# Kernel optimization log

Measured on AMD Instinct MI355X. Metric: run time of the kernel, lower is better.

The kernel has to match this reference:

```python
import jax, jax.numpy as jnp
import numpy as np

N, E, F, H, O, B = 100000, 1200000, 64, 1024, 1, 256


def _gcn_conv(x, W, b, src, dst, ew, num_nodes):
    # PyG GCNConv: out_i = sum_{(s->i)} d_i^{-1/2} w_e d_s^{-1/2} (x_s W) + b
    deg = jax.ops.segment_sum(ew, dst, num_segments=num_nodes)
    dinv = jnp.where(deg > 0, jax.lax.rsqrt(jnp.maximum(deg, 1e-12)), 0.0)
    norm = dinv[src] * ew * dinv[dst]          # [E]
    h = x @ W                                   # [N, out]
    msg = h[src] * norm[:, None]                # gather + scale
    return jax.ops.segment_sum(msg, dst, num_segments=num_nodes) + b


def setup_inputs() -> dict:
    key = jax.random.key(0)
    ks = jax.random.split(key, 12)
    def lin(k, fan_in, fan_out):
        s = 1.0 / np.sqrt(fan_in)
        kw, kb = jax.random.split(k)
        return (jax.random.uniform(kw, (fan_in, fan_out), jnp.float32, -s, s),
                jax.random.uniform(kb, (fan_out,), jnp.float32, -s, s))
    W1, b1 = lin(ks[0], F, F)
    W2, b2 = lin(ks[1], F, 2 * F)
    W3, b3 = lin(ks[2], 2 * F, 4 * F)
    Wf1, bf1 = lin(ks[3], 5 * F, H)
    Wf2, bf2 = lin(ks[4], H, O)
    feature = jax.random.normal(ks[5], (N, F), jnp.float32)
    edge_index = jax.random.randint(ks[6], (2, E), 0, N, jnp.int32)
    weight = jax.random.uniform(ks[7], (E,), jnp.float32)
    protein_batch = jnp.sort(jax.random.randint(ks[8], (N,), 0, B, jnp.int32))
    return {"feature": feature, "edge_index": edge_index, "weight": weight,
            "protein_batch": protein_batch,
            "W1": W1, "b1": b1, "W2": W2, "b2": b2, "W3": W3, "b3": b3,
            "Wf1": Wf1, "bf1": bf1, "Wf2": Wf2, "bf2": bf2}


def reference(feature, edge_index, weight, protein_batch,
              W1, b1, W2, b2, W3, b3, Wf1, bf1, Wf2, bf2):
    num_nodes = feature.shape[0]
    # add self-loops with weight 1 (PyG default)
    loop = jnp.arange(num_nodes, dtype=edge_index.dtype)
    src = jnp.concatenate([edge_index[0], loop])
    dst = jnp.concatenate([edge_index[1], loop])
    ew = jnp.concatenate([weight, jnp.ones((num_nodes,), weight.dtype)])

    x = jax.nn.relu(_gcn_conv(feature, W1, b1, src, dst, ew, num_nodes))
    x = jax.nn.relu(_gcn_conv(x, W2, b2, src, dst, ew, num_nodes))
    x = jax.nn.relu(_gcn_conv(x, W3, b3, src, dst, ew, num_nodes))
    x = jnp.concatenate([x, feature], axis=1)   # [N, 5F]

    # global_mean_pool over graph ids
    sums = jax.ops.segment_sum(x, protein_batch, num_segments=B)
    cnts = jax.ops.segment_sum(jnp.ones((num_nodes,), x.dtype), protein_batch, num_segments=B)
    gc = sums / jnp.maximum(cnts, 1.0)[:, None]

    gc = jax.nn.relu(gc @ Wf1 + bf1)            # dropout is identity in eval
    return gc @ Wf2 + bf2
```

## Files before the change

kernel.cpp:

```cpp
#include <hip/hip_runtime.h>
#include <cstdio>
#include <cstdint>

typedef _Float16 f16x8 __attribute__((ext_vector_type(8)));
typedef float f32x4 __attribute__((ext_vector_type(4)));

__device__ inline unsigned short f2bf(float f) {
  unsigned u = __float_as_uint(f);
  u += 0x7fffu + ((u >> 16) & 1u);
  return (unsigned short)(u >> 16);
}
__device__ inline float bf2f(unsigned short h) {
  return __uint_as_float(((unsigned)h) << 16);
}
__device__ inline unsigned short f2h(float f) {
  union { _Float16 h; unsigned short u; } cv;
  cv.h = (_Float16)f;
  return cv.u;
}

#define EPB 4096


__global__ __launch_bounds__(256)
void k_prep0(float* __restrict__ psum,
             const float* __restrict__ feature, ushort* __restrict__ featb,
             const float* __restrict__ W1, ushort* __restrict__ w1h,
             const float* __restrict__ W2, ushort* __restrict__ w2h,
             const float* __restrict__ W3, ushort* __restrict__ w3h,
             const int* __restrict__ pb, int* __restrict__ gs,
             const int* __restrict__ dst, int* __restrict__ H,
             int* __restrict__ rs,
             int BC, int NF, int F, int D2, int D3,
             int N, int B, int NB, int E,
             int nB, int nC, int nD, int nG) {
  __shared__ int hist[512];
  int b = blockIdx.x;
  int t = threadIdx.x;
  if (b < nB) {
    int i = b * 256 + t;
    if (i < BC) psum[i] = 0.f;
  } else if (b < nB + nC) {
    int base = ((b - nB) * 256 + t) * 4;
    if (base < NF) {
      float4 v = *reinterpret_cast<const float4*>(feature + base);
      ushort4 h;
      h.x = f2bf(v.x); h.y = f2bf(v.y); h.z = f2bf(v.z); h.w = f2bf(v.w);
      *reinterpret_cast<ushort4*>(featb + base) = h;
    }
  } else if (b < nB + nC + nD) {
    int idx = (b - nB - nC) * 256 + t;
    int s1 = F * F, s2 = s1 + F * D2, s3 = s2 + D2 * D3;
    if (idx < s1) {
      int k = idx / F, n = idx - k * F;
      w1h[(size_t)n * F + k] = f2h(W1[idx]);
    } else if (idx < s2) {
      int i2 = idx - s1; int k = i2 / D2, n = i2 - k * D2;
      w2h[(size_t)n * F + k] = f2h(W2[i2]);
    } else if (idx < s3) {
      int i3 = idx - s2; int k = i3 / D3, n = i3 - k * D3;
      w3h[(size_t)n * D2 + k] = f2h(W3[i3]);
    }
  } else if (b < nB + nC + nD + nG) {
    int bb = (b - nB - nC - nD) * 256 + t;
    if (bb == 0) rs[N] = E;
    if (bb <= B) {
      int lo = 0, hi = N;
      while (lo < hi) {
        int mid = (lo + hi) >> 1;
        if (pb[mid] < bb) lo = mid + 1; else hi = mid;
      }
      gs[bb] = lo;
    }
  } else {
    const int bi = b - nB - nC - nD - nG;
    for (int i = t; i < NB; i += 256) hist[i] = 0;
    __syncthreads();
    const int base = bi * EPB + t;
#pragma unroll
    for (int j = 0; j < EPB / 256; j++) {
      int e = base + 256 * j;
      if (e < E) atomicAdd(&hist[dst[e] >> 8], 1);
    }
    __syncthreads();
    for (int i = t; i < NB; i += 256) H[(size_t)bi * NB + i] = hist[i];
  }
}

__global__ __launch_bounds__(256)
void k_bscan1(const int* __restrict__ H, int* __restrict__ S,
              int* __restrict__ bsum, int NB, int NBLK, int T) {
  __shared__ int sh[256];
  const int t = threadIdx.x;
  const int base = blockIdx.x * 1024;
  int v[4]; int s = 0;
#pragma unroll
  for (int j = 0; j < 4; j++) {
    int idx = base + t * 4 + j;
    if (idx < T) {
      int bin = idx / NBLK, bi = idx - bin * NBLK;
      v[j] = H[(size_t)bi * NB + bin];
    } else v[j] = 0;
    s += v[j];
  }
  sh[t] = s;
  __syncthreads();
  for (int off = 1; off < 256; off <<= 1) {
    int x = (t >= off) ? sh[t - off] : 0;
    __syncthreads();
    sh[t] += x;
    __syncthreads();
  }
  int run = sh[t] - s;
#pragma unroll
  for (int j = 0; j < 4; j++) {
    int idx = base + t * 4 + j;
    if (idx < T) S[idx] = run;
    run += v[j];
  }
  if (t == 255) bsum[blockIdx.x] = sh[255];
}

__device__ inline void build_prefix(const int* __restrict__ bsum, int nch,
                                    int* __restrict__ pre, int t) {
  for (int i = t; i < nch; i += 256) pre[i] = bsum[i];
  __syncthreads();
  if (t == 0) {
    int run = 0;
    for (int i = 0; i < nch; i++) { int v = pre[i]; pre[i] = run; run += v; }
  }
  __syncthreads();
}

__global__ __launch_bounds__(256)
void k_bscatter(const int* __restrict__ src, const int* __restrict__ dst,
                const float* __restrict__ ew, const int* __restrict__ S,
                const int* __restrict__ bsb,
                int* __restrict__ sdst, int2* __restrict__ ssw,
                int NB, int NBLK, int E, int nchT) {
  __shared__ int cnt[512];
  __shared__ int sbase[512];
  __shared__ int pre[512];
  const int t = threadIdx.x, bi = blockIdx.x;
  build_prefix(bsb, nchT, pre, t);
  for (int i = t; i < NB; i += 256) {
    cnt[i] = 0;
    int j = i * NBLK + bi;
    sbase[i] = S[j] + pre[j >> 10];
  }
  __syncthreads();
  const int base = bi * EPB + t;
#pragma unroll
  for (int j = 0; j < EPB / 256; j++) {
    int e = base + 256 * j;
    if (e < E) {
      int d = dst[e];
      int bin = d >> 8;
      int r = atomicAdd(&cnt[bin], 1);
      int pos = sbase[bin] + r;
      sdst[pos] = d;
      ssw[pos] = make_int2(src[e], __float_as_int(ew[e]));
    }
  }
}

__global__ __launch_bounds__(256)
void k_bprocA(const int* __restrict__ sdst, const int2* __restrict__ ssw,
              const int* __restrict__ S, const int* __restrict__ bsb,
              int* __restrict__ cntN, float* __restrict__ wsumN,
              int NB, int NBLK, int N, int E, int nchT) {
  __shared__ int cnt[256];
  __shared__ float wsm[256];
  __shared__ int pre[512];
  const int t = threadIdx.x, bin = blockIdx.x;
  build_prefix(bsb, nchT, pre, t);
  cnt[t] = 0; wsm[t] = 0.f;
  __syncthreads();
  int j0 = bin * NBLK;
  const int start = S[j0] + pre[j0 >> 10];
  int end = E;
  if (bin + 1 < NB) { int j1 = (bin + 1) * NBLK; end = S[j1] + pre[j1 >> 10]; }
  for (int p = start + t; p < end; p += 256) {
    int ld = sdst[p] & 255;
    atomicAdd(&cnt[ld], 1);
    atomicAdd(&wsm[ld], __int_as_float(ssw[p].y));
  }
  __syncthreads();
  int n = bin * 256 + t;
  if (n < N) { cntN[n] = cnt[t]; wsumN[n] = wsm[t]; }
}

__global__ __launch_bounds__(256)
void k_scan1(const int* __restrict__ cntN, const float* __restrict__ wsumN,
             int* __restrict__ rs, int* __restrict__ bsum,
             float* __restrict__ dinv, float* __restrict__ sn, int N) {
  __shared__ int sh[256];
  const int t = threadIdx.x;
  const int base = blockIdx.x * 1024;
  int v[4]; int s = 0;
#pragma unroll
  for (int j = 0; j < 4; j++) {
    int idx = base + t * 4 + j;
    if (idx < N) {
      v[j] = cntN[idx];
      double deg = 1.0 + (double)wsumN[idx];
      float r = (float)(1.0 / sqrt(deg));
      dinv[idx] = r;
      sn[idx] = r * r;
    } else v[j] = 0;
    s += v[j];
  }
  sh[t] = s;
  __syncthreads();
  for (int off = 1; off < 256; off <<= 1) {
    int x = (t >= off) ? sh[t - off] : 0;
    __syncthreads();
    sh[t] += x;
    __syncthreads();
  }
  int run = sh[t] - s;
#pragma unroll
  for (int j = 0; j < 4; j++) {
    int idx = base + t * 4 + j;
    if (idx < N) rs[idx] = run;
    run += v[j];
  }
  if (t == 255) bsum[blockIdx.x] = sh[255];
}

__global__ __launch_bounds__(256)
void k_bprocB(const int* __restrict__ sdst, const int2* __restrict__ ssw,
              const int* __restrict__ S, const int* __restrict__ bsb,
              int* __restrict__ rs, const int* __restrict__ bsumN,
              const float* __restrict__ dinv,
              int2* __restrict__ epack,
              int NB, int NBLK, int N, int E, int nchT, int nchN) {
  __shared__ int cnt[256];
  __shared__ float sdv[256];
  __shared__ int srs[256];
  __shared__ int preT[512];
  __shared__ int preN[128];
  const int t = threadIdx.x, bin = blockIdx.x;
  for (int i = t; i < nchT; i += 256) preT[i] = bsb[i];
  for (int i = t; i < nchN; i += 256) preN[i] = bsumN[i];
  __syncthreads();
  if (t == 0) {
    int run = 0;
    for (int i = 0; i < nchT; i++) { int v = preT[i]; preT[i] = run; run += v; }
    run = 0;
    for (int i = 0; i < nchN; i++) { int v = preN[i]; preN[i] = run; run += v; }
  }
  __syncthreads();
  cnt[t] = 0;
  int n = bin * 256 + t;
  sdv[t] = (n < N) ? dinv[n] : 0.f;
  int rabs = 0;
  if (n < N) {
    rabs = rs[n] + preN[n >> 10];
    rs[n] = rabs;
  }
  srs[t] = rabs;
  __syncthreads();
  int j0 = bin * NBLK;
  const int start = S[j0] + preT[j0 >> 10];
  int end = E;
  if (bin + 1 < NB) { int j1 = (bin + 1) * NBLK; end = S[j1] + preT[j1 >> 10]; }
  for (int p = start + t; p < end; p += 256) {
    int d = sdst[p];
    int ld = d & 255;
    int2 sw = ssw[p];
    int r = atomicAdd(&cnt[ld], 1);
    float w = dinv[sw.x] * __int_as_float(sw.y) * sdv[ld];
    epack[srs[ld] + r] = make_int2(sw.x, __float_as_int(w));
  }
}


__device__ inline void bf8_fma(const int4 v, float w, float* acc) {
  acc[0] = fmaf(__uint_as_float((unsigned)v.x << 16), w, acc[0]);
  acc[1] = fmaf(__uint_as_float((unsigned)v.x & 0xffff0000u), w, acc[1]);
  acc[2] = fmaf(__uint_as_float((unsigned)v.y << 16), w, acc[2]);
  acc[3] = fmaf(__uint_as_float((unsigned)v.y & 0xffff0000u), w, acc[3]);
  acc[4] = fmaf(__uint_as_float((unsigned)v.z << 16), w, acc[4]);
  acc[5] = fmaf(__uint_as_float((unsigned)v.z & 0xffff0000u), w, acc[5]);
  acc[6] = fmaf(__uint_as_float((unsigned)v.w << 16), w, acc[6]);
  acc[7] = fmaf(__uint_as_float((unsigned)v.w & 0xffff0000u), w, acc[7]);
}

template<int LOG2L>
__global__ __launch_bounds__(256)
void k_aggregate_b(const ushort* __restrict__ Xb, const int* __restrict__ rs,
                   const int2* __restrict__ epack, const float* __restrict__ sn,
                   ushort* __restrict__ AH, int N) {
  const int t = blockIdx.x * blockDim.x + threadIdx.x;
  const int row = t >> LOG2L;
  if (row >= N) return;
  const int L = 1 << LOG2L;
  const int D = L << 3;
  const int c = (t & (L - 1)) << 3;
  const ushort* __restrict__ Xc = Xb + c;

  float acc[8];
  {
    int4 v = *reinterpret_cast<const int4*>(Xc + (size_t)row * D);
    float s = sn[row];
    acc[0] = s * __uint_as_float((unsigned)v.x << 16);
    acc[1] = s * __uint_as_float((unsigned)v.x & 0xffff0000u);
    acc[2] = s * __uint_as_float((unsigned)v.y << 16);
    acc[3] = s * __uint_as_float((unsigned)v.y & 0xffff0000u);
    acc[4] = s * __uint_as_float((unsigned)v.z << 16);
    acc[5] = s * __uint_as_float((unsigned)v.z & 0xffff0000u);
    acc[6] = s * __uint_as_float((unsigned)v.w << 16);
    acc[7] = s * __uint_as_float((unsigned)v.w & 0xffff0000u);
  }
  const int p0 = rs[row], pe = rs[row + 1];
  int i = p0;
  if ((i & 1) && i < pe) {
    int2 e = epack[i];
    int4 v = *reinterpret_cast<const int4*>(Xc + (size_t)e.x * D);
    bf8_fma(v, __int_as_float(e.y), acc);
    i++;
  }
  for (; i + 8 <= pe; i += 8) {
    int4 ea = *reinterpret_cast<const int4*>(&epack[i]);
    int4 eb = *reinterpret_cast<const int4*>(&epack[i + 2]);
    int4 ec = *reinterpret_cast<const int4*>(&epack[i + 4]);
    int4 ed = *reinterpret_cast<const int4*>(&epack[i + 6]);
    int4 v0 = *reinterpret_cast<const int4*>(Xc + (size_t)ea.x * D);
    int4 v1 = *reinterpret_cast<const int4*>(Xc + (size_t)ea.z * D);
    int4 v2 = *reinterpret_cast<const int4*>(Xc + (size_t)eb.x * D);
    int4 v3 = *reinterpret_cast<const int4*>(Xc + (size_t)eb.z * D);
    int4 v4 = *reinterpret_cast<const int4*>(Xc + (size_t)ec.x * D);
    int4 v5 = *reinterpret_cast<const int4*>(Xc + (size_t)ec.z * D);
    int4 v6 = *reinterpret_cast<const int4*>(Xc + (size_t)ed.x * D);
    int4 v7 = *reinterpret_cast<const int4*>(Xc + (size_t)ed.z * D);
    bf8_fma(v0, __int_as_float(ea.y), acc);
    bf8_fma(v1, __int_as_float(ea.w), acc);
    bf8_fma(v2, __int_as_float(eb.y), acc);
    bf8_fma(v3, __int_as_float(eb.w), acc);
    bf8_fma(v4, __int_as_float(ec.y), acc);
    bf8_fma(v5, __int_as_float(ec.w), acc);
    bf8_fma(v6, __int_as_float(ed.y), acc);
    bf8_fma(v7, __int_as_float(ed.w), acc);
  }
  if (i + 4 <= pe) {
    int4 ea = *reinterpret_cast<const int4*>(&epack[i]);
    int4 eb = *reinterpret_cast<const int4*>(&epack[i + 2]);
    int4 v0 = *reinterpret_cast<const int4*>(Xc + (size_t)ea.x * D);
    int4 v1 = *reinterpret_cast<const int4*>(Xc + (size_t)ea.z * D);
    int4 v2 = *reinterpret_cast<const int4*>(Xc + (size_t)eb.x * D);
    int4 v3 = *reinterpret_cast<const int4*>(Xc + (size_t)eb.z * D);
    bf8_fma(v0, __int_as_float(ea.y), acc);
    bf8_fma(v1, __int_as_float(ea.w), acc);
    bf8_fma(v2, __int_as_float(eb.y), acc);
    bf8_fma(v3, __int_as_float(eb.w), acc);
    i += 4;
  }
  if (i + 2 <= pe) {
    int4 e2 = *reinterpret_cast<const int4*>(&epack[i]);
    int4 v0 = *reinterpret_cast<const int4*>(Xc + (size_t)e2.x * D);
    int4 v1 = *reinterpret_cast<const int4*>(Xc + (size_t)e2.z * D);
    bf8_fma(v0, __int_as_float(e2.y), acc);
    bf8_fma(v1, __int_as_float(e2.w), acc);
    i += 2;
  }
  if (i < pe) {
    int2 e = epack[i];
    int4 v = *reinterpret_cast<const int4*>(Xc + (size_t)e.x * D);
    bf8_fma(v, __int_as_float(e.y), acc);
  }
  ushort h[8];
#pragma unroll
  for (int j = 0; j < 8; j++) h[j] = f2h(acc[j]);
  size_t o = (size_t)row * D + c;
  *reinterpret_cast<ushort4*>(AH + o)     = make_ushort4(h[0], h[1], h[2], h[3]);
  *reinterpret_cast<ushort4*>(AH + o + 4) = make_ushort4(h[4], h[5], h[6], h[7]);
}


template<int KT, int TPB>
__global__ __launch_bounds__(256, 3)
void k_gemm_rb(const ushort* __restrict__ Ah, const ushort* __restrict__ Bh,
               const float* __restrict__ bias, ushort* __restrict__ Y,
               int N, int D) {
  constexpr int NT = 64;
  constexpr int NK = KT / 32;
  const int t = threadIdx.x;
  const int wave = t >> 6, lane = t & 63;
  const int quad = lane >> 4, l16 = lane & 15;
  const int n0 = blockIdx.x * NT;
  const int mbase = blockIdx.y * (TPB * 128);

  f16x8 bf[NK][4];
#pragma unroll
  for (int k0 = 0; k0 < NK; k0++)
#pragma unroll
    for (int ni = 0; ni < 4; ni++)
      bf[k0][ni] = *reinterpret_cast<const f16x8*>(
          Bh + (size_t)(n0 + ni * 16 + l16) * KT + k0 * 32 + quad * 8);

  float bv[4];
#pragma unroll
  for (int ni = 0; ni < 4; ni++) bv[ni] = bias[n0 + ni * 16 + l16];

#pragma unroll 1
  for (int tile = 0; tile < TPB; tile++) {
    const int rt = mbase + tile * 128 + wave * 32 + l16;
    if (mbase + tile * 128 >= N) break;
    int r0 = rt;      if (r0 >= N) r0 = N - 1;
    int r1 = rt + 16; if (r1 >= N) r1 = N - 1;
    const ushort* __restrict__ A0 = Ah + (size_t)r0 * KT + quad * 8;
    const ushort* __restrict__ A1 = Ah + (size_t)r1 * KT + quad * 8;

    f16x8 a0[NK], a1[NK];
#pragma unroll
    for (int k0 = 0; k0 < NK; k0++) {
      a0[k0] = *reinterpret_cast<const f16x8*>(A0 + k0 * 32);
      a1[k0] = *reinterpret_cast<const f16x8*>(A1 + k0 * 32);
    }

    f32x4 acc[2][4];
#pragma unroll
    for (int mi = 0; mi < 2; mi++)
#pragma unroll
      for (int ni = 0; ni < 4; ni++) acc[mi][ni] = (f32x4){0.f, 0.f, 0.f, 0.f};

#pragma unroll
    for (int k0 = 0; k0 < NK; k0++)
#pragma unroll
      for (int ni = 0; ni < 4; ni++) {
        acc[0][ni] = __builtin_amdgcn_mfma_f32_16x16x32_f16(a0[k0], bf[k0][ni], acc[0][ni], 0, 0, 0);
        acc[1][ni] = __builtin_amdgcn_mfma_f32_16x16x32_f16(a1[k0], bf[k0][ni], acc[1][ni], 0, 0, 0);
      }

    const int rb0 = mbase + tile * 128 + wave * 32 + quad * 4;
#pragma unroll
    for (int mi = 0; mi < 2; mi++) {
      int rb = rb0 + mi * 16;
#pragma unroll
      for (int ni = 0; ni < 4; ni++) {
        int col = n0 + ni * 16 + l16;
#pragma unroll
        for (int r = 0; r < 4; r++) {
          int row = rb + r;
          if (row < N)
            Y[(size_t)row * D + col] = f2bf(fmaxf(acc[mi][ni][r] + bv[ni], 0.f));
        }
      }
    }
  }
}


#define PSPLIT 4

__global__ void k_pool(const ushort* __restrict__ X3b, const float* __restrict__ feat,
                       const int* __restrict__ gs, float* __restrict__ psum,
                       int D3, int F) {
  const int c = threadIdx.x;
  const int C = D3 + F;
  const int b = blockIdx.y;
  const int sp = blockIdx.x;
  const int s0 = gs[b], e0 = gs[b + 1];
  const int len = e0 - s0;
  if (len <= 0) return;
  const int chunk = (len + PSPLIT - 1) / PSPLIT;
  const int s = s0 + sp * chunk;
  int e = s + chunk; if (e > e0) e = e0;
  if (s >= e) return;
  const int n = e - s;
  float a0 = 0.f, a1 = 0.f, a2 = 0.f, a3 = 0.f;
  float a4 = 0.f, a5 = 0.f, a6 = 0.f, a7 = 0.f;
  if (c < D3) {
    const ushort* p = X3b + (size_t)s * D3 + c;
    int i = 0;
    for (; i + 8 <= n; i += 8) {
      a0 += bf2f(p[0 * (size_t)D3]);
      a1 += bf2f(p[1 * (size_t)D3]);
      a2 += bf2f(p[2 * (size_t)D3]);
      a3 += bf2f(p[3 * (size_t)D3]);
      a4 += bf2f(p[4 * (size_t)D3]);
      a5 += bf2f(p[5 * (size_t)D3]);
      a6 += bf2f(p[6 * (size_t)D3]);
      a7 += bf2f(p[7 * (size_t)D3]);
      p += 8 * (size_t)D3;
    }
    for (; i < n; i++) { a0 += bf2f(*p); p += D3; }
  } else {
    const float* p = feat + (size_t)s * F + (c - D3);
    int i = 0;
    for (; i + 8 <= n; i += 8) {
      a0 += p[0 * (size_t)F];
      a1 += p[1 * (size_t)F];
      a2 += p[2 * (size_t)F];
      a3 += p[3 * (size_t)F];
      a4 += p[4 * (size_t)F];
      a5 += p[5 * (size_t)F];
      a6 += p[6 * (size_t)F];
      a7 += p[7 * (size_t)F];
      p += 8 * (size_t)F;
    }
    for (; i < n; i++) { a0 += *p; p += F; }
  }
  float tot = ((a0 + a1) + (a2 + a3)) + ((a4 + a5) + (a6 + a7));
  atomicAdd(&psum[(size_t)b * C + c], tot);
}


__global__ __launch_bounds__(256)
void k_fc1(const float* __restrict__ psum, const int* __restrict__ gs,
           const float* __restrict__ Wf1, const float* __restrict__ bf1,
           float* __restrict__ hidden, int C, int Hh) {
  const int b = blockIdx.y;
  __shared__ float gcs[384];
  float invc = 1.f / fmaxf((float)(gs[b + 1] - gs[b]), 1.f);
  for (int c = threadIdx.x; c < C; c += 256)
    gcs[c] = psum[(size_t)b * C + c] * invc;
  __syncthreads();
  const int j = blockIdx.x * 256 + threadIdx.x;
  if (j >= Hh) return;
  const float* w = Wf1 + j;
  float a0 = 0.f, a1 = 0.f, a2 = 0.f, a3 = 0.f;
  int c = 0;
  for (; c + 4 <= C; c += 4) {
    a0 = fmaf(gcs[c + 0], w[(size_t)(c + 0) * Hh], a0);
    a1 = fmaf(gcs[c + 1], w[(size_t)(c + 1) * Hh], a1);
    a2 = fmaf(gcs[c + 2], w[(size_t)(c + 2) * Hh], a2);
    a3 = fmaf(gcs[c + 3], w[(size_t)(c + 3) * Hh], a3);
  }
  for (; c < C; c++) a0 = fmaf(gcs[c], w[(size_t)c * Hh], a0);
  float r = ((a0 + a1) + (a2 + a3)) + bf1[j];
  hidden[(size_t)b * Hh + j] = fmaxf(r, 0.f);
}

__global__ void k_fc2(const float* __restrict__ hidden, const float* __restrict__ Wf2,
                      const float* __restrict__ bf2, float* __restrict__ out, int Hh) {
  int b = blockIdx.x;
  int lane = threadIdx.x;
  double s = 0.0;
  for (int j = lane; j < Hh; j += 64) s += (double)hidden[(size_t)b * Hh + j] * (double)Wf2[j];
#pragma unroll
  for (int off = 32; off > 0; off >>= 1) s += __shfl_down(s, off);
  if (lane == 0) out[b] = (float)s + bf2[0];
}


extern "C" void kernel_launch(void* const* d_in, const int* in_sizes, int n_in,
                              void* d_out, int out_size, void* d_ws, size_t ws_size,
                              hipStream_t stream) {
  const float* feature = (const float*)d_in[0];
  const int*   eidx    = (const int*)  d_in[1];
  const float* weight  = (const float*)d_in[2];
  const int*   pb      = (const int*)  d_in[3];
  const float* W1  = (const float*)d_in[4];
  const float* b1  = (const float*)d_in[5];
  const float* W2  = (const float*)d_in[6];
  const float* b2  = (const float*)d_in[7];
  const float* W3  = (const float*)d_in[8];
  const float* b3  = (const float*)d_in[9];
  const float* Wf1 = (const float*)d_in[10];
  const float* bf1 = (const float*)d_in[11];
  const float* Wf2 = (const float*)d_in[12];
  const float* bf2 = (const float*)d_in[13];

  const int F  = in_sizes[5];
  const int D2 = in_sizes[7];
  const int D3 = in_sizes[9];
  const int Hh = in_sizes[11];
  const int N  = in_sizes[0] / F;
  const int E  = in_sizes[1] / 2;
  const int B  = out_size;
  const int C  = D3 + F;

  const int* srcp = eidx;
  const int* dstp = eidx + E;

  const int NB   = (N + 255) / 256;
  const int NBLK = (E + EPB - 1) / EPB;
  const int T    = NB * NBLK;
  const int nchT = (T + 1023) / 1024;
  const int nchN = (N + 1023) / 1024;

  auto al = [](size_t x) { return (x + 255) & ~(size_t)255; };
  size_t off = 0;
  auto alloc = [&](size_t bytes) { size_t o = off; off += al(bytes); return o; };
  size_t o_H     = alloc((size_t)T * 4);
  size_t o_S     = alloc((size_t)T * 4);
  size_t o_bsb   = alloc((size_t)nchT * 4);
  size_t o_sdst  = alloc((size_t)E * 4);
  size_t o_ssw   = alloc((size_t)E * 8);
  size_t o_cntN  = alloc((size_t)N * 4);
  size_t o_wsumN = alloc((size_t)N * 4);
  size_t o_dinv  = alloc((size_t)N * 4);
  size_t o_sn    = alloc((size_t)N * 4);
  size_t o_rs    = alloc((size_t)(N + 1) * 4);
  size_t o_bsum  = alloc((size_t)nchN * 4);
  size_t o_epack = alloc((size_t)E * 8);
  size_t o_featb = alloc((size_t)N * F  * 2);
  size_t o_x1b   = alloc((size_t)N * F  * 2);
  size_t o_x2b   = alloc((size_t)N * D2 * 2);
  size_t o_x3b   = alloc((size_t)N * D3 * 2);
  size_t o_aggh  = alloc((size_t)N * D2 * 2);
  size_t o_w1h   = alloc((size_t)F  * F  * 2);
  size_t o_w2h   = alloc((size_t)F  * D2 * 2);
  size_t o_w3h   = alloc((size_t)D2 * D3 * 2);
  size_t o_psum  = alloc((size_t)B * C * 4);
  size_t o_gs    = alloc((size_t)(B + 1) * 4);
  size_t o_hid   = alloc((size_t)B * Hh * 4);
  if (off > ws_size) {
    fprintf(stderr, "kernel_launch: workspace too small: need %zu, have %zu\n", off, ws_size);
    return;
  }

  char* ws = (char*)d_ws;
  int*    H     = (int*)  (ws + o_H);
  int*    S     = (int*)  (ws + o_S);
  int*    bsb   = (int*)  (ws + o_bsb);
  int*    sdst  = (int*)  (ws + o_sdst);
  int2*   ssw   = (int2*) (ws + o_ssw);
  int*    cntN  = (int*)  (ws + o_cntN);
  float*  wsumN = (float*)(ws + o_wsumN);
  float*  dinv  = (float*)(ws + o_dinv);
  float*  sn    = (float*)(ws + o_sn);
  int*    rs    = (int*)  (ws + o_rs);
  int*    bsum  = (int*)  (ws + o_bsum);
  int2*   epack = (int2*) (ws + o_epack);
  ushort* featb = (ushort*)(ws + o_featb);
  ushort* x1b   = (ushort*)(ws + o_x1b);
  ushort* x2b   = (ushort*)(ws + o_x2b);
  ushort* x3b   = (ushort*)(ws + o_x3b);
  ushort* aggh  = (ushort*)(ws + o_aggh);
  ushort* w1h   = (ushort*)(ws + o_w1h);
  ushort* w2h   = (ushort*)(ws + o_w2h);
  ushort* w3h   = (ushort*)(ws + o_w3h);
  float*  psum  = (float*) (ws + o_psum);
  int*    gs    = (int*)  (ws + o_gs);
  float*  hid   = (float*)(ws + o_hid);
  float*  out   = (float*)d_out;

  const int BC = B * C, NF = N * F;
  const int nB = (BC + 255) / 256;
  const int nC = (NF / 4 + 255) / 256;
  const int nD = (F * F + F * D2 + D2 * D3 + 255) / 256;
  const int nG = (B + 1 + 255) / 256;
  k_prep0<<<nB + nC + nD + nG + NBLK, 256, 0, stream>>>(
      psum, feature, featb, W1, w1h, W2, w2h, W3, w3h,
      pb, gs, dstp, H, rs,
      BC, NF, F, D2, D3, N, B, NB, E, nB, nC, nD, nG);

  k_bscan1  <<<nchT, 256, 0, stream>>>(H, S, bsb, NB, NBLK, T);
  k_bscatter<<<NBLK, 256, 0, stream>>>(srcp, dstp, weight, S, bsb, sdst, ssw, NB, NBLK, E, nchT);
  k_bprocA  <<<NB, 256, 0, stream>>>(sdst, ssw, S, bsb, cntN, wsumN, NB, NBLK, N, E, nchT);
  k_scan1   <<<nchN, 256, 0, stream>>>(cntN, wsumN, rs, bsum, dinv, sn, N);
  k_bprocB  <<<NB, 256, 0, stream>>>(sdst, ssw, S, bsb, rs, bsum, dinv, epack, NB, NBLK, N, E, nchT, nchN);

  const int Mt = (N + 127) / 128;

  {
    int tot = N * (F / 8);
    k_aggregate_b<3><<<(tot + 255) / 256, 256, 0, stream>>>(featb, rs, epack, sn, aggh, N);
    dim3 g(1, Mt);
    k_gemm_rb<64, 1><<<g, 256, 0, stream>>>(aggh, w1h, b1, x1b, N, F);
  }
  {
    int tot = N * (F / 8);
    k_aggregate_b<3><<<(tot + 255) / 256, 256, 0, stream>>>(x1b, rs, epack, sn, aggh, N);
    dim3 g(2, (Mt + 1) / 2);
    k_gemm_rb<64, 2><<<g, 256, 0, stream>>>(aggh, w2h, b2, x2b, N, D2);
  }
  {
    int tot = N * (D2 / 8);
    k_aggregate_b<4><<<(tot + 255) / 256, 256, 0, stream>>>(x2b, rs, epack, sn, aggh, N);
    dim3 g(4, (Mt + 3) / 4);
    k_gemm_rb<128, 4><<<g, 256, 0, stream>>>(aggh, w3h, b3, x3b, N, D3);
  }

  {
    dim3 g(PSPLIT, B);
    k_pool<<<g, C, 0, stream>>>(x3b, feature, gs, psum, D3, F);
  }
  {
    dim3 g((Hh + 255) / 256, B);
    k_fc1<<<g, 256, 0, stream>>>(psum, gs, Wf1, bf1, hid, C, Hh);
  }
  k_fc2  <<<B, 64, 0, stream>>>(hid, Wf2, bf2, out, Hh);
}
```

Before: 392.1 us.

## Fuse neighbor aggregation with MFMA GEMM via shared-memory tile per layer

Merges the per-layer aggregation kernel and the GEMM kernel into one kernel. Each block aggregates 128 rows into a padded LDS tile in fp16, then four waves each compute a slice of the output columns with MFMA straight from LDS. This removes the global write and read of the intermediate aggregated matrix and three kernel launches. In exchange the gather phase now runs with a fixed block-wide LDS footprint and a barrier before the GEMM, and the weights are reloaded per block.

```diff
diff --git a/kernel.cpp b/kernel.cpp
--- a/kernel.cpp
+++ b/kernel.cpp
@@ -287,20 +287,12 @@
   acc[7] = fmaf(__uint_as_float((unsigned)v.w & 0xffff0000u), w, acc[7]);
 }
 
-template<int LOG2L>
-__global__ __launch_bounds__(256)
-void k_aggregate_b(const ushort* __restrict__ Xb, const int* __restrict__ rs,
-                   const int2* __restrict__ epack, const float* __restrict__ sn,
-                   ushort* __restrict__ AH, int N) {
-  const int t = blockIdx.x * blockDim.x + threadIdx.x;
-  const int row = t >> LOG2L;
-  if (row >= N) return;
-  const int L = 1 << LOG2L;
-  const int D = L << 3;
-  const int c = (t & (L - 1)) << 3;
-  const ushort* __restrict__ Xc = Xb + c;
-
-  float acc[8];
+template<int D>
+__device__ inline void agg_row(const ushort* __restrict__ Xc,
+                               const int* __restrict__ rs,
+                               const int2* __restrict__ epack,
+                               const float* __restrict__ sn,
+                               int row, float* __restrict__ acc) {
   {
     int4 v = *reinterpret_cast<const int4*>(Xc + (size_t)row * D);
     float s = sn[row];
@@ -369,82 +361,98 @@
     int4 v = *reinterpret_cast<const int4*>(Xc + (size_t)e.x * D);
     bf8_fma(v, __int_as_float(e.y), acc);
   }
-  ushort h[8];
-#pragma unroll
-  for (int j = 0; j < 8; j++) h[j] = f2h(acc[j]);
-  size_t o = (size_t)row * D + c;
-  *reinterpret_cast<ushort4*>(AH + o)     = make_ushort4(h[0], h[1], h[2], h[3]);
-  *reinterpret_cast<ushort4*>(AH + o + 4) = make_ushort4(h[4], h[5], h[6], h[7]);
-}
-
-
-template<int KT, int TPB>
-__global__ __launch_bounds__(256, 3)
-void k_gemm_rb(const ushort* __restrict__ Ah, const ushort* __restrict__ Bh,
-               const float* __restrict__ bias, ushort* __restrict__ Y,
-               int N, int D) {
-  constexpr int NT = 64;
+}
+
+
+template<int KT, int DT>
+__global__ __launch_bounds__(256)
+void k_agg_gemm(const ushort* __restrict__ Xb, const int* __restrict__ rs,
+                const int2* __restrict__ epack, const float* __restrict__ sn,
+                const ushort* __restrict__ Bh, const float* __restrict__ bias,
+                ushort* __restrict__ Y, int N) {
+  constexpr int PK = KT + 8;
+  constexpr int L = KT / 8;
+  constexpr int RPP = 256 / L;
+  constexpr int NPASS = 128 / RPP;
+  constexpr int NTW = DT / 4;
+  constexpr int NF = NTW / 16;
   constexpr int NK = KT / 32;
+  __shared__ __align__(16) ushort sA[128 * PK];
   const int t = threadIdx.x;
+  const int m0 = blockIdx.x * 128;
+
+  {
+    const int rloc0 = t / L;
+    const int c = (t & (L - 1)) << 3;
+    const ushort* __restrict__ Xc = Xb + c;
+#pragma unroll 1
+    for (int pass = 0; pass < NPASS; pass++) {
+      const int rloc = pass * RPP + rloc0;
+      const int row = m0 + rloc;
+      float acc[8];
+      if (row < N) {
+        agg_row<KT>(Xc, rs, epack, sn, row, acc);
+      } else {
+#pragma unroll
+        for (int j = 0; j < 8; j++) acc[j] = 0.f;
+      }
+      ushort h[8];
+#pragma unroll
+      for (int j = 0; j < 8; j++) h[j] = f2h(acc[j]);
+      *reinterpret_cast<ushort4*>(&sA[rloc * PK + c])     = make_ushort4(h[0], h[1], h[2], h[3]);
+      *reinterpret_cast<ushort4*>(&sA[rloc * PK + c + 4]) = make_ushort4(h[4], h[5], h[6], h[7]);
+    }
+  }
+  __syncthreads();
+
   const int wave = t >> 6, lane = t & 63;
   const int quad = lane >> 4, l16 = lane & 15;
-  const int n0 = blockIdx.x * NT;
-  const int mbase = blockIdx.y * (TPB * 128);
-
-  f16x8 bf[NK][4];
+  const int n0 = wave * NTW;
+
+  f16x8 bf[NK][NF];
 #pragma unroll
   for (int k0 = 0; k0 < NK; k0++)
 #pragma unroll
-    for (int ni = 0; ni < 4; ni++)
+    for (int ni = 0; ni < NF; ni++)
       bf[k0][ni] = *reinterpret_cast<const f16x8*>(
           Bh + (size_t)(n0 + ni * 16 + l16) * KT + k0 * 32 + quad * 8);
 
-  float bv[4];
-#pragma unroll
-  for (int ni = 0; ni < 4; ni++) bv[ni] = bias[n0 + ni * 16 + l16];
-
-#pragma unroll 1
-  for (int tile = 0; tile < TPB; tile++) {
-    const int rt = mbase + tile * 128 + wave * 32 + l16;
-    if (mbase + tile * 128 >= N) break;
-    int r0 = rt;      if (r0 >= N) r0 = N - 1;
-    int r1 = rt + 16; if (r1 >= N) r1 = N - 1;
-    const ushort* __restrict__ A0 = Ah + (size_t)r0 * KT + quad * 8;
-    const ushort* __restrict__ A1 = Ah + (size_t)r1 * KT + quad * 8;
-
+  float bv[NF];
+#pragma unroll
+  for (int ni = 0; ni < NF; ni++) bv[ni] = bias[n0 + ni * 16 + l16];
+
+#pragma unroll
+  for (int ms = 0; ms < 4; ms++) {
+    const int r0 = ms * 32 + l16;
     f16x8 a0[NK], a1[NK];
 #pragma unroll
     for (int k0 = 0; k0 < NK; k0++) {
-      a0[k0] = *reinterpret_cast<const f16x8*>(A0 + k0 * 32);
-      a1[k0] = *reinterpret_cast<const f16x8*>(A1 + k0 * 32);
-    }
-
-    f32x4 acc[2][4];
+      a0[k0] = *reinterpret_cast<const f16x8*>(&sA[r0 * PK + k0 * 32 + quad * 8]);
+      a1[k0] = *reinterpret_cast<const f16x8*>(&sA[(r0 + 16) * PK + k0 * 32 + quad * 8]);
+    }
+    f32x4 acc[2][NF];
 #pragma unroll
     for (int mi = 0; mi < 2; mi++)
 #pragma unroll
-      for (int ni = 0; ni < 4; ni++) acc[mi][ni] = (f32x4){0.f, 0.f, 0.f, 0.f};
-
+      for (int ni = 0; ni < NF; ni++) acc[mi][ni] = (f32x4){0.f, 0.f, 0.f, 0.f};
 #pragma unroll
     for (int k0 = 0; k0 < NK; k0++)
 #pragma unroll
-      for (int ni = 0; ni < 4; ni++) {
+      for (int ni = 0; ni < NF; ni++) {
         acc[0][ni] = __builtin_amdgcn_mfma_f32_16x16x32_f16(a0[k0], bf[k0][ni], acc[0][ni], 0, 0, 0);
         acc[1][ni] = __builtin_amdgcn_mfma_f32_16x16x32_f16(a1[k0], bf[k0][ni], acc[1][ni], 0, 0, 0);
       }
-
-    const int rb0 = mbase + tile * 128 + wave * 32 + quad * 4;
 #pragma unroll
     for (int mi = 0; mi < 2; mi++) {
-      int rb = rb0 + mi * 16;
-#pragma unroll
-      for (int ni = 0; ni < 4; ni++) {
-        int col = n0 + ni * 16 + l16;
+      const int rb = m0 + ms * 32 + mi * 16 + quad * 4;
+#pragma unroll
+      for (int ni = 0; ni < NF; ni++) {
+        const int col = n0 + ni * 16 + l16;
 #pragma unroll
         for (int r = 0; r < 4; r++) {
           int row = rb + r;
           if (row < N)
-            Y[(size_t)row * D + col] = f2bf(fmaxf(acc[mi][ni][r] + bv[ni], 0.f));
+            Y[(size_t)row * DT + col] = f2bf(fmaxf(acc[mi][ni][r] + bv[ni], 0.f));
         }
       }
     }
@@ -600,7 +608,6 @@
   size_t o_x1b   = alloc((size_t)N * F  * 2);
   size_t o_x2b   = alloc((size_t)N * D2 * 2);
   size_t o_x3b   = alloc((size_t)N * D3 * 2);
-  size_t o_aggh  = alloc((size_t)N * D2 * 2);
   size_t o_w1h   = alloc((size_t)F  * F  * 2);
   size_t o_w2h   = alloc((size_t)F  * D2 * 2);
   size_t o_w3h   = alloc((size_t)D2 * D3 * 2);
@@ -629,7 +636,6 @@
   ushort* x1b   = (ushort*)(ws + o_x1b);
   ushort* x2b   = (ushort*)(ws + o_x2b);
   ushort* x3b   = (ushort*)(ws + o_x3b);
-  ushort* aggh  = (ushort*)(ws + o_aggh);
   ushort* w1h   = (ushort*)(ws + o_w1h);
   ushort* w2h   = (ushort*)(ws + o_w2h);
   ushort* w3h   = (ushort*)(ws + o_w3h);
@@ -656,24 +662,9 @@
 
   const int Mt = (N + 127) / 128;
 
-  {
-    int tot = N * (F / 8);
-    k_aggregate_b<3><<<(tot + 255) / 256, 256, 0, stream>>>(featb, rs, epack, sn, aggh, N);
-    dim3 g(1, Mt);
-    k_gemm_rb<64, 1><<<g, 256, 0, stream>>>(aggh, w1h, b1, x1b, N, F);
-  }
-  {
-    int tot = N * (F / 8);
-    k_aggregate_b<3><<<(tot + 255) / 256, 256, 0, stream>>>(x1b, rs, epack, sn, aggh, N);
-    dim3 g(2, (Mt + 1) / 2);
-    k_gemm_rb<64, 2><<<g, 256, 0, stream>>>(aggh, w2h, b2, x2b, N, D2);
-  }
-  {
-    int tot = N * (D2 / 8);
-    k_aggregate_b<4><<<(tot + 255) / 256, 256, 0, stream>>>(x2b, rs, epack, sn, aggh, N);
-    dim3 g(4, (Mt + 3) / 4);
-    k_gemm_rb<128, 4><<<g, 256, 0, stream>>>(aggh, w3h, b3, x3b, N, D3);
-  }
+  k_agg_gemm<64,  64><<<Mt, 256, 0, stream>>>(featb, rs, epack, sn, w1h, b1, x1b, N);
+  k_agg_gemm<64, 128><<<Mt, 256, 0, stream>>>(x1b,   rs, epack, sn, w2h, b2, x2b, N);
+  k_agg_gemm<128,256><<<Mt, 256, 0, stream>>>(x2b,   rs, epack, sn, w3h, b3, x3b, N);
 
   {
     dim3 g(PSPLIT, B);
```

After: 396.5 us. No clear change (+1.1%).
